# Kernel optimization log

Hardware: AMD Instinct MI355X
Metric: run time of the kernel (lower is better)

Reference implementation:

```python
import jax, jax.numpy as jnp
import numpy as np

B, I, H, R = 8192, 512, 1024, 64  # batch, input_size, hidden_size, rank (w_rank == u_ranks[-1])


def setup_inputs() -> dict:
    key = jax.random.key(0)
    ks = jax.random.split(key, 11)
    f = jax.random.normal
    return {
        "x": f(ks[0], (B, I), jnp.float32),
        "h": f(ks[1], (B, H), jnp.float32),
        "c": f(ks[2], (B, H), jnp.float32),
        "u_x": 0.1 * f(ks[3], (I, R), jnp.float32),
        "u_h": 0.1 * f(ks[4], (H, R), jnp.float32),
        "v_x": 0.1 * f(ks[5], (4 * H, R), jnp.float32),
        "v_h": 0.1 * f(ks[6], (4 * H, R), jnp.float32),
        "b_x": 0.1 * f(ks[7], (4 * H,), jnp.float32),
        "b_h": 0.1 * f(ks[8], (4 * H,), jnp.float32),
        "dia_x": 0.1 * f(ks[9], (1, I), jnp.float32),
        "dia_h": 0.1 * f(ks[10], (1, H), jnp.float32),
    }


def reference(x, h, c, u_x, u_h, v_x, v_h, b_x, b_h, dia_x, dia_h):
    Bn = x.shape[0]
    # diagonal (vector-multiplication) terms; vm_x padded to hidden size (H >= I)
    vm_x = jnp.pad(dia_x * x, ((0, 0), (0, H - I)))          # [B, H]
    vm_h = dia_h * h                                          # [B, H]
    # low-rank projections: [B,R] @ [R,4H]
    lowered_x = (x @ u_x) @ v_x.T                             # [B, 4H]
    lowered_h = (h @ u_h) @ v_h.T                             # [B, 4H]
    # vectorized form of the 4-gate refinement loop
    v_x4 = v_x.reshape(4, H, R)
    v_h4 = v_h.reshape(4, H, R)
    coef_x = jnp.sum(u_x[None] * v_x4[:, :I, :], axis=-1)    # [4, I]
    coef_h = jnp.sum(u_h[None] * v_h4, axis=-1)              # [4, H]
    ref_x = jnp.pad(x[:, None, :] * coef_x[None], ((0, 0), (0, 0), (0, H - I))).reshape(Bn, 4 * H)
    ref_h = (h[:, None, :] * coef_h[None]).reshape(Bn, 4 * H)
    gx = lowered_x - ref_x + b_x
    gh = lowered_h - ref_h + b_h
    xi, xf, xo, xn = jnp.split(gx, 4, axis=1)
    hi, hf, ho, hn = jnp.split(gh, 4, axis=1)
    z = vm_x + vm_h
    inputgate = jax.nn.sigmoid(xi + hi + z)
    forgetgate = jax.nn.sigmoid(xf + hf + z)
    outputgate = jax.nn.sigmoid(xo + ho + z)
    newgate = jnp.tanh(xn + hn + z)
    c_next = forgetgate * c + inputgate * newgate
    h_next = outputgate * jnp.tanh(c_next)
    return h_next, c_next
```

## Files before the change

### kernel.cpp

```cpp
#include <hip/hip_runtime.h>
#include <hip/hip_bf16.h>

#define B_ 8192
#define I_ 512
#define H_ 1024
#define R_ 64

typedef __bf16 bf16x8 __attribute__((ext_vector_type(8)));
typedef short  s16x8  __attribute__((ext_vector_type(8)));
typedef float  f32x4  __attribute__((ext_vector_type(4)));

static __device__ __forceinline__ short f2bf(float f) {
    union { float f; unsigned u; } v; v.f = f;
    unsigned r = v.u + 0x7fffu + ((v.u >> 16) & 1u);
    return (short)(r >> 16);
}
static __device__ __forceinline__ float frcp_(float x) {
#if __has_builtin(__builtin_amdgcn_rcpf)
    return __builtin_amdgcn_rcpf(x);
#else
    float r; asm("v_rcp_f32 %0, %1" : "=v"(r) : "v"(x)); return r;
#endif
}
static __device__ __forceinline__ float sigmoidf_(float v) {
    return frcp_(1.f + __expf(-v));
}
static __device__ __forceinline__ float tanhf_(float v) {
    return 2.f * frcp_(1.f + __expf(-2.f * v)) - 1.f;
}

__global__ __launch_bounds__(256) void prep_kernel(
    const float* __restrict__ u_x, const float* __restrict__ u_h,
    const float* __restrict__ v_x, const float* __restrict__ v_h,
    short* __restrict__ uxT, short* __restrict__ uhT, short* __restrict__ Vc,
    float* __restrict__ coef_x, float* __restrict__ coef_h)
{
    int t = blockIdx.x * 256 + threadIdx.x;
    if (t < 64 * 512) {
        int k = t >> 6, r = t & 63;
        uxT[r * 512 + k] = f2bf(u_x[t]);
        return;
    }
    t -= 64 * 512;
    if (t < 64 * 1024) {
        int k = t >> 6, r = t & 63;
        uhT[r * 1024 + k] = f2bf(u_h[t]);
        return;
    }
    t -= 64 * 1024;
    if (t < 4096 * 128) {
        int n = t >> 7, q = t & 127;
        Vc[t] = f2bf(q < 64 ? v_x[n * 64 + q] : v_h[n * 64 + (q - 64)]);
        return;
    }
    t -= 4096 * 128;
    if (t < 1536 * 64) {
        const int wid = t >> 6, lane = t & 63;
        const float* U; const float* V; float* C; int j, JN;
        if (wid < 512) { U = u_x; V = v_x; C = coef_x; j = wid;       JN = 512;  }
        else           { U = u_h; V = v_h; C = coef_h; j = wid - 512; JN = 1024; }
        const float uv = U[(size_t)j * 64 + lane];
        float s[4];
#pragma unroll
        for (int g = 0; g < 4; ++g)
            s[g] = uv * V[(size_t)(g * H_ + j) * 64 + lane];
#pragma unroll
        for (int off = 32; off >= 1; off >>= 1)
#pragma unroll
            for (int g = 0; g < 4; ++g)
                s[g] += __shfl_xor(s[g], off, 64);
        if (lane == 0)
#pragma unroll
            for (int g = 0; g < 4; ++g)
                C[g * JN + j] = s[g];
        return;
    }
}

__global__ __launch_bounds__(256) void stage1_kernel(
    const float* __restrict__ x, const float* __restrict__ h,
    const short* __restrict__ uxT, const short* __restrict__ uhT,
    short* __restrict__ P)
{
    __shared__ short At[16 * 136];
    const int w = threadIdx.x >> 6, lane = threadIdx.x & 63;
    const int quad = lane >> 4, lr = lane & 15;
    const int n0 = w * 16;

    const float* X; const short* UT; int K, co;
    if (blockIdx.y == 0) { X = x; UT = uxT; K = I_; co = 0; }
    else                 { X = h; UT = uhT; K = H_; co = 64; }

    const int b0 = blockIdx.x * 16;
    const int srow = threadIdx.x >> 4;
    const int scol = (threadIdx.x & 15) * 8;

    f32x4 acc = {};
    const short* bp = UT + (size_t)(n0 + lr) * K + quad * 8;
    const short* arow = At + lr * 136 + quad * 8;
    const float* srcbase = X + (size_t)(b0 + srow) * K + scol;

    float4 c0 = ((const float4*)(srcbase))[0];
    float4 c1 = ((const float4*)(srcbase))[1];

    for (int k0 = 0; k0 < K; k0 += 128) {
        s16x8 p;
        p[0] = f2bf(c0.x); p[1] = f2bf(c0.y); p[2] = f2bf(c0.z); p[3] = f2bf(c0.w);
        p[4] = f2bf(c1.x); p[5] = f2bf(c1.y); p[6] = f2bf(c1.z); p[7] = f2bf(c1.w);
        __syncthreads();
        *(s16x8*)(At + srow * 136 + scol) = p;
        __syncthreads();
        if (k0 + 128 < K) {
            c0 = ((const float4*)(srcbase + k0 + 128))[0];
            c1 = ((const float4*)(srcbase + k0 + 128))[1];
        }
#pragma unroll
        for (int ks = 0; ks < 4; ++ks) {
            bf16x8 bfrag = *(const bf16x8*)(bp + k0 + ks * 32);
            bf16x8 afrag = *(const bf16x8*)(arow + ks * 32);
            acc = __builtin_amdgcn_mfma_f32_16x16x32_bf16(afrag, bfrag, acc, 0, 0, 0);
        }
    }

#pragma unroll
    for (int r = 0; r < 4; ++r)
        P[(size_t)(b0 + quad * 4 + r) * 128 + co + n0 + lr] = f2bf(acc[r]);
}

__global__ __launch_bounds__(256) void stage2_kernel(
    const short* __restrict__ P, const short* __restrict__ Vc,
    const float* __restrict__ x, const float* __restrict__ h,
    const float* __restrict__ c,
    const float* __restrict__ coef_x, const float* __restrict__ coef_h,
    const float* __restrict__ b_x, const float* __restrict__ b_h,
    const float* __restrict__ dia_x, const float* __restrict__ dia_h,
    float* __restrict__ out)
{
    const int lane = threadIdx.x & 63;
    const int wv   = threadIdx.x >> 6;
    const int quad = lane >> 4, lr = lane & 15;
    const int b0 = blockIdx.x * 128;
    const int j0 = blockIdx.y * 64 + wv * 16;
    const int j = j0 + lr;
    const bool jx = (j < I_);

    bf16x8 bfr[4][4];
#pragma unroll
    for (int g = 0; g < 4; ++g)
#pragma unroll
        for (int ks = 0; ks < 4; ++ks)
            bfr[g][ks] = *(const bf16x8*)(Vc + (size_t)(g * H_ + j0 + lr) * 128 + ks * 32 + quad * 8);

    const float dx = jx ? dia_x[j] : 0.f;
    const float dh = dia_h[j];
    float cx[4], ch[4], bsum[4];
#pragma unroll
    for (int g = 0; g < 4; ++g) {
        cx[g]   = jx ? coef_x[g * I_ + j] : 0.f;
        ch[g]   = coef_h[g * H_ + j];
        bsum[g] = b_x[g * H_ + j] + b_h[g * H_ + j];
    }

    bf16x8 a[4];
#pragma unroll
    for (int ks = 0; ks < 4; ++ks)
        a[ks] = *(const bf16x8*)(P + (size_t)(b0 + lr) * 128 + ks * 32 + quad * 8);
    float xv[4], hv[4], cv[4];
#pragma unroll
    for (int r = 0; r < 4; ++r) {
        const int brow = b0 + quad * 4 + r;
        cv[r] = c[(size_t)brow * H_ + j];
        hv[r] = h[(size_t)brow * H_ + j];
        xv[r] = jx ? x[(size_t)brow * I_ + j] : 0.f;
    }

    for (int mt = 0; mt < 8; ++mt) {
        bf16x8 an[4];
        float xn[4], hn[4], cn2[4];
        if (mt < 7) {
            const int rb = b0 + (mt + 1) * 16;
#pragma unroll
            for (int ks = 0; ks < 4; ++ks)
                an[ks] = *(const bf16x8*)(P + (size_t)(rb + lr) * 128 + ks * 32 + quad * 8);
#pragma unroll
            for (int r = 0; r < 4; ++r) {
                const int brow = rb + quad * 4 + r;
                cn2[r] = c[(size_t)brow * H_ + j];
                hn[r]  = h[(size_t)brow * H_ + j];
                xn[r]  = jx ? x[(size_t)brow * I_ + j] : 0.f;
            }
        }

        f32x4 acc[4] = {};
#pragma unroll
        for (int ks = 0; ks < 4; ++ks)
#pragma unroll
            for (int g = 0; g < 4; ++g)
                acc[g] = __builtin_amdgcn_mfma_f32_16x16x32_bf16(a[ks], bfr[g][ks], acc[g], 0, 0, 0);

#pragma unroll
        for (int r = 0; r < 4; ++r) {
            const int brow = b0 + mt * 16 + quad * 4 + r;
            const float xe = xv[r], he = hv[r];
            const float z  = dx * xe + dh * he;

            const float g0 = acc[0][r] - xe * cx[0] - he * ch[0] + bsum[0] + z;
            const float g1 = acc[1][r] - xe * cx[1] - he * ch[1] + bsum[1] + z;
            const float g2 = acc[2][r] - xe * cx[2] - he * ch[2] + bsum[2] + z;
            const float g3 = acc[3][r] - xe * cx[3] - he * ch[3] + bsum[3] + z;

            const float ig = sigmoidf_(g0);
            const float fg = sigmoidf_(g1);
            const float og = sigmoidf_(g2);
            const float ng = tanhf_(g3);

            const float cn = fg * cv[r] + ig * ng;
            const float hnv = og * tanhf_(cn);

            out[(size_t)brow * H_ + j] = hnv;
            out[(size_t)B_ * H_ + (size_t)brow * H_ + j] = cn;
        }

        if (mt < 7) {
#pragma unroll
            for (int ks = 0; ks < 4; ++ks) a[ks] = an[ks];
#pragma unroll
            for (int r = 0; r < 4; ++r) { xv[r] = xn[r]; hv[r] = hn[r]; cv[r] = cn2[r]; }
        }
    }
}

extern "C" void kernel_launch(void* const* d_in, const int* in_sizes, int n_in,
                              void* d_out, int out_size, void* d_ws, size_t ws_size,
                              hipStream_t stream) {
    const float* x     = (const float*)d_in[0];
    const float* h     = (const float*)d_in[1];
    const float* c     = (const float*)d_in[2];
    const float* u_x   = (const float*)d_in[3];
    const float* u_h   = (const float*)d_in[4];
    const float* v_x   = (const float*)d_in[5];
    const float* v_h   = (const float*)d_in[6];
    const float* b_x   = (const float*)d_in[7];
    const float* b_h   = (const float*)d_in[8];
    const float* dia_x = (const float*)d_in[9];
    const float* dia_h = (const float*)d_in[10];
    float* out = (float*)d_out;

    char* ws = (char*)d_ws;
    short* P      = (short*)(ws);
    short* uxT    = (short*)(ws + 2097152);
    short* uhT    = (short*)(ws + 2097152 + 65536);
    short* Vc     = (short*)(ws + 2097152 + 65536 + 131072);
    float* coef_x = (float*)(ws + 2097152 + 65536 + 131072 + 1048576);
    float* coef_h = (float*)(ws + 2097152 + 65536 + 131072 + 1048576 + 8192);

    prep_kernel<<<2816, 256, 0, stream>>>(u_x, u_h, v_x, v_h, uxT, uhT, Vc, coef_x, coef_h);
    stage1_kernel<<<dim3(512, 2), 256, 0, stream>>>(x, h, uxT, uhT, P);
    stage2_kernel<<<dim3(64, 16), 256, 0, stream>>>(P, Vc, x, h, c,
                                                    coef_x, coef_h, b_x, b_h,
                                                    dia_x, dia_h, out);
}
```

Before: 192.8 us.

## Stage elementwise loads and stores through double-buffered LDS for 16-byte global access

In stage2, x/h/c tiles are now loaded cooperatively as float4 rows into double-buffered shared memory, and h_next/c_next results are staged in LDS and written back as float4 rows one iteration later. Before, each lane did scalar 4-byte strided accesses in the MFMA fragment layout. The goal is wider, fully coalesced global transactions. The cost is a __syncthreads per tile, extra LDS traffic and about 43 KB of shared memory per block, which may lower occupancy.

```diff
diff --git a/kernel.cpp b/kernel.cpp
--- a/kernel.cpp
+++ b/kernel.cpp
@@ -136,13 +136,33 @@
     const float* __restrict__ dia_x, const float* __restrict__ dia_h,
     float* __restrict__ out)
 {
-    const int lane = threadIdx.x & 63;
-    const int wv   = threadIdx.x >> 6;
+    __shared__ float inx[2][16 * 68];
+    __shared__ float inh[2][16 * 68];
+    __shared__ float inc[2][16 * 68];
+    __shared__ float oh_[2][16 * 68];
+    __shared__ float oc_[2][16 * 68];
+
+    const int tid  = threadIdx.x;
+    const int lane = tid & 63,  wv = tid >> 6;
     const int quad = lane >> 4, lr = lane & 15;
-    const int b0 = blockIdx.x * 128;
-    const int j0 = blockIdx.y * 64 + wv * 16;
-    const int j = j0 + lr;
-    const bool jx = (j < I_);
+    const int b0  = blockIdx.x * 128;
+    const int j0b = blockIdx.y * 64;
+    const int j0  = j0b + wv * 16;
+    const int j   = j0 + lr;
+    const bool jx = (j0b < I_);
+
+    const int srow = tid >> 4;
+    const int scol = (tid & 15) * 4;
+    const int sidx = srow * 68 + scol;
+    const int jl   = wv * 16 + lr;
+
+    f32x4 sx = {}, sh, sc;
+    {
+        const int gr = b0 + srow;
+        sc = *(const f32x4*)(c + (size_t)gr * H_ + j0b + scol);
+        sh = *(const f32x4*)(h + (size_t)gr * H_ + j0b + scol);
+        if (jx) sx = *(const f32x4*)(x + (size_t)gr * I_ + j0b + scol);
+    }
 
     bf16x8 bfr[4][4];
 #pragma unroll
@@ -165,31 +185,13 @@
 #pragma unroll
     for (int ks = 0; ks < 4; ++ks)
         a[ks] = *(const bf16x8*)(P + (size_t)(b0 + lr) * 128 + ks * 32 + quad * 8);
-    float xv[4], hv[4], cv[4];
-#pragma unroll
-    for (int r = 0; r < 4; ++r) {
-        const int brow = b0 + quad * 4 + r;
-        cv[r] = c[(size_t)brow * H_ + j];
-        hv[r] = h[(size_t)brow * H_ + j];
-        xv[r] = jx ? x[(size_t)brow * I_ + j] : 0.f;
-    }
+
+    *(f32x4*)&inc[0][sidx] = sc;
+    *(f32x4*)&inh[0][sidx] = sh;
+    if (jx) *(f32x4*)&inx[0][sidx] = sx;
 
     for (int mt = 0; mt < 8; ++mt) {
-        bf16x8 an[4];
-        float xn[4], hn[4], cn2[4];
-        if (mt < 7) {
-            const int rb = b0 + (mt + 1) * 16;
-#pragma unroll
-            for (int ks = 0; ks < 4; ++ks)
-                an[ks] = *(const bf16x8*)(P + (size_t)(rb + lr) * 128 + ks * 32 + quad * 8);
-#pragma unroll
-            for (int r = 0; r < 4; ++r) {
-                const int brow = rb + quad * 4 + r;
-                cn2[r] = c[(size_t)brow * H_ + j];
-                hn[r]  = h[(size_t)brow * H_ + j];
-                xn[r]  = jx ? x[(size_t)brow * I_ + j] : 0.f;
-            }
-        }
+        const int buf = mt & 1;
 
         f32x4 acc[4] = {};
 #pragma unroll
@@ -198,10 +200,35 @@
             for (int g = 0; g < 4; ++g)
                 acc[g] = __builtin_amdgcn_mfma_f32_16x16x32_bf16(a[ks], bfr[g][ks], acc[g], 0, 0, 0);
 
+        __syncthreads();
+
+        bf16x8 an[4];
+        if (mt < 7) {
+            const int gr = b0 + (mt + 1) * 16 + srow;
+            sc = *(const f32x4*)(c + (size_t)gr * H_ + j0b + scol);
+            sh = *(const f32x4*)(h + (size_t)gr * H_ + j0b + scol);
+            if (jx) sx = *(const f32x4*)(x + (size_t)gr * I_ + j0b + scol);
+            const int rb = b0 + (mt + 1) * 16 + lr;
+#pragma unroll
+            for (int ks = 0; ks < 4; ++ks)
+                an[ks] = *(const bf16x8*)(P + (size_t)rb * 128 + ks * 32 + quad * 8);
+        }
+
+        if (mt > 0) {
+            const int gr = b0 + (mt - 1) * 16 + srow;
+            const int pb = (mt - 1) & 1;
+            f32x4 vh = *(const f32x4*)&oh_[pb][sidx];
+            f32x4 vc = *(const f32x4*)&oc_[pb][sidx];
+            *(f32x4*)(out + (size_t)gr * H_ + j0b + scol) = vh;
+            *(f32x4*)(out + (size_t)B_ * H_ + (size_t)gr * H_ + j0b + scol) = vc;
+        }
+
 #pragma unroll
         for (int r = 0; r < 4; ++r) {
-            const int brow = b0 + mt * 16 + quad * 4 + r;
-            const float xe = xv[r], he = hv[r];
+            const int rl = quad * 4 + r;
+            const float xe = jx ? inx[buf][rl * 68 + jl] : 0.f;
+            const float he = inh[buf][rl * 68 + jl];
+            const float ce = inc[buf][rl * 68 + jl];
             const float z  = dx * xe + dh * he;
 
             const float g0 = acc[0][r] - xe * cx[0] - he * ch[0] + bsum[0] + z;
@@ -214,19 +241,29 @@
             const float og = sigmoidf_(g2);
             const float ng = tanhf_(g3);
 
-            const float cn = fg * cv[r] + ig * ng;
+            const float cn  = fg * ce + ig * ng;
             const float hnv = og * tanhf_(cn);
 
-            out[(size_t)brow * H_ + j] = hnv;
-            out[(size_t)B_ * H_ + (size_t)brow * H_ + j] = cn;
+            oh_[buf][rl * 68 + jl] = hnv;
+            oc_[buf][rl * 68 + jl] = cn;
         }
 
         if (mt < 7) {
+            *(f32x4*)&inc[buf ^ 1][sidx] = sc;
+            *(f32x4*)&inh[buf ^ 1][sidx] = sh;
+            if (jx) *(f32x4*)&inx[buf ^ 1][sidx] = sx;
 #pragma unroll
             for (int ks = 0; ks < 4; ++ks) a[ks] = an[ks];
-#pragma unroll
-            for (int r = 0; r < 4; ++r) { xv[r] = xn[r]; hv[r] = hn[r]; cv[r] = cn2[r]; }
-        }
+        }
+    }
+
+    __syncthreads();
+    {
+        const int gr = b0 + 7 * 16 + srow;
+        f32x4 vh = *(const f32x4*)&oh_[1][sidx];
+        f32x4 vc = *(const f32x4*)&oc_[1][sidx];
+        *(f32x4*)(out + (size_t)gr * H_ + j0b + scol) = vh;
+        *(f32x4*)(out + (size_t)B_ * H_ + (size_t)gr * H_ + j0b + scol) = vc;
     }
 }
 
```

Measured after the change: 184.7 us. 4.2% less time.
